# Optimization experiments

Measured on AMD Instinct MI355X. Metric: run time of the kernel, lower is better.

Reference implementation:

```python
import jax, jax.numpy as jnp
import numpy as np

F_FILT = 40      # num_filters
K_GABOR = 401    # n_coefficients
K_POOL = 401     # window_length
HOP = 160        # hop_length
SR = 16000
EPS_PCEN = 1e-6
EPS_IN = 1e-5    # nn.InstanceNorm1d default eps
B, T = 8, 160000


def _hz2mel(f):
    return 2595.0 * np.log10(1.0 + f / 700.0)


def _mel2hz(m):
    return 700.0 * (10.0 ** (m / 2595.0) - 1.0)


def setup_inputs() -> dict:
    key = jax.random.key(0)
    x = jax.random.normal(key, (B, 1, T), dtype=jnp.float32)
    # mel-spaced Gabor center frequencies / bandwidths (filter_init_method='mel')
    edges = _mel2hz(np.linspace(_hz2mel(60.0), _hz2mel(7800.0), F_FILT + 2))
    center = edges[1:-1]
    fwhm = np.maximum(edges[2:] - edges[:-2], 1.0)
    eta = 2.0 * np.pi * center / SR                      # rad/sample
    sigma = np.sqrt(2.0 * np.log(2.0)) / (np.pi * fwhm / SR)  # samples
    ones = jnp.ones(F_FILT, jnp.float32)
    return {
        "x": x,
        "gabor_eta": jnp.asarray(eta, jnp.float32),
        "gabor_sigma": jnp.asarray(sigma, jnp.float32),
        "pool_bandwidths": 0.4 * ones,   # GaussianLowPass init
        "pool_bias": ones,               # GaussianLowPass bias init (ones)
        "ema_weights": 0.04 * ones,      # sPCEN smoothing_coefficient, per-channel
        "alpha": 0.96 * ones,
        "delta": 2.0 * ones,
        "root": 0.96 * ones,             # root=compression_factor=0.96
    }


def _conv1d(x, w, stride=1, groups=1):
    # x: (N, C, T), w: (O, C//groups, K); cross-correlation like torch F.conv1d
    return jax.lax.conv_general_dilated(
        x, w, (stride,), "VALID",
        dimension_numbers=("NCH", "OIH", "NCH"),
        feature_group_count=groups)


def _ema_scan(x, s):
    # y_0 = x_0 ; y_t = s*x_t + (1-s)*y_{t-1}  (per-channel s), parallel scan
    s3 = s[None, :, None]
    a = jnp.broadcast_to(1.0 - s3, x.shape)
    b = s3 * x
    a = a.at[:, :, 0].set(0.0)
    b = b.at[:, :, 0].set(x[:, :, 0])
    def comb(c1, c2):
        a1, b1 = c1
        a2, b2 = c2
        return a1 * a2, a2 * b1 + b2
    _, y = jax.lax.associative_scan(comb, (a, b), axis=2)
    return y


def reference(x, gabor_eta, gabor_sigma, pool_bandwidths, pool_bias,
              ema_weights, alpha, delta, root):
    dt = x.dtype
    # --- Gabor complex conv frontend -> |.|^2 ---
    t = jnp.arange(K_GABOR, dtype=dt) - (K_GABOR - 1) / 2.0
    env = jnp.exp(-0.5 * (t[None] / gabor_sigma[:, None]) ** 2) \
          / (jnp.sqrt(2.0 * jnp.pi) * gabor_sigma[:, None])
    phase = gabor_eta[:, None] * t[None]
    kern = jnp.stack([env * jnp.cos(phase), env * jnp.sin(phase)], axis=1)
    kern = kern.reshape(2 * F_FILT, 1, K_GABOR)
    xp = jnp.pad(x, ((0, 0), (0, 0), (K_GABOR - 1, 0)))  # causal pad
    y = _conv1d(xp, kern)                                 # (B, 2F, T)
    y = y.reshape(y.shape[0], F_FILT, 2, y.shape[-1])
    power = y[:, :, 0] ** 2 + y[:, :, 1] ** 2             # |z|^2, (B, F, T)

    # --- sPCEN compression ---
    s = jnp.clip(ema_weights, 0.0, 1.0)
    ema = _ema_scan(power, s)
    a3 = jnp.minimum(alpha, 1.0)[None, :, None]
    inv_r = (1.0 / jnp.maximum(root, 1.0))[None, :, None]
    d3 = delta[None, :, None]
    comp = (power / (EPS_PCEN + ema) ** a3 + d3) ** inv_r - d3 ** inv_r

    # --- Gaussian low-pass depthwise pooling (causal, stride=HOP) ---
    bw = jnp.clip(pool_bandwidths, 2.0 / K_POOL, 0.5)
    tp = jnp.arange(-K_POOL // 2, K_POOL // 2, dtype=dt)  # -201..199, len 401
    den = bw * 0.5 * (K_POOL - 1)
    pk = jnp.exp(-0.5 * (tp[None] / den[:, None]) ** 2).reshape(F_FILT, 1, K_POOL)
    cp = jnp.pad(comp, ((0, 0), (0, 0), (K_POOL - 1, 0)))
    pooled = _conv1d(cp, pk, stride=HOP, groups=F_FILT) + pool_bias[None, :, None]

    # --- InstanceNorm1d (affine=False, biased var, eps=1e-5) ---
    m = pooled.mean(-1, keepdims=True)
    v = pooled.var(-1, keepdims=True)
    return (pooled - m) / jnp.sqrt(v + EPS_IN)
```

## Files before the change

### kernel.cpp

```cpp
#include <hip/hip_runtime.h>
#include <math.h>

#define F_FILT   40
#define K_GABOR  401
#define HOP      160
#define T_LEN    160000
#define B_BATCH  8
#define EPS_PCENF 1e-6f
#define EPS_INF   1e-5f

#define NG       5
#define GF       8
#define NKMAX    13
#define TC       640
#define UW       10
#define NCH1     250
#define NSTG     136
#define PHS      548

#define PC_THREADS 256
#define PC_NWAVES  4
#define SPAN     6400
#define W_NT     5
#define NSP      25
#define RT       20
#define KP       208
#define HALOP    200
#define RINGW    840
#define WSTR     1048

typedef _Float16 h2_t  __attribute__((ext_vector_type(2)));
typedef _Float16 half8 __attribute__((ext_vector_type(8)));
typedef float    f32x4 __attribute__((ext_vector_type(4)));

__device__ __forceinline__ float fdot2(h2_t a, h2_t b, float c) {
    return __builtin_amdgcn_fdot2(a, b, c, false);
}
__device__ __forceinline__ unsigned pk2(float a, float b) {
    return __builtin_bit_cast(unsigned, __builtin_amdgcn_cvt_pkrtz(a, b));
}
__device__ __forceinline__ h2_t bch(unsigned u) {
    return __builtin_bit_cast(h2_t, u);
}
__device__ __forceinline__ float fexp2(float x) { return __builtin_amdgcn_exp2f(x); }
__device__ __forceinline__ float flog2(float x) { return __builtin_amdgcn_logf(x); }

__device__ __forceinline__ void group_span(float sigma0, int& klo, int& nk) {
    const int R = min(200, (int)ceilf(4.0f * sigma0));
    klo = (200 - R) & ~31;
    nk  = ((200 + R - klo) >> 5) + 1;
    if (nk > NKMAX) nk = NKMAX;
}

__global__ __launch_bounds__(256) void leaf_weights(
    const float* __restrict__ eta_g, const float* __restrict__ sigma_g,
    const float* __restrict__ bw_g,
    _Float16* __restrict__ Atab, unsigned* __restrict__ pktab)
{
    const int gi = blockIdx.x;
    const int f0 = gi * GF;
    int klo, nk;
    group_span(sigma_g[f0], klo, nk);

    for (int idx = threadIdx.x; idx < 52 * 16 * 8; idx += 256) {
        const int c8 = idx >> 7;
        const int m  = (idx >> 3) & 15;
        const int i  = idx & 7;
        const int f  = f0 + (m >> 1);
        const int k  = klo + c8 * 8 + i;
        float w = 0.f;
        if (k <= 400) {
            const float sg = sigma_g[f];
            const float t  = (float)(k - 200);
            const float z  = t / sg;
            const float e  = (0.3989422804014327f / sg) * expf(-0.5f * z * z);
            const float ph = eta_g[f] * t;
            w = (m & 1) ? e * sinf(ph) : e * cosf(ph);
        }
        Atab[(size_t)(gi * 52 + c8) * 128 + m * 8 + i] = (_Float16)w;
    }
    for (int idx = threadIdx.x; idx < GF * KP; idx += 256) {
        const int fl = idx / KP, i = idx % KP;
        const int f = f0 + fl;
        const float bw  = fminf(fmaxf(bw_g[f], 2.0f / 401.0f), 0.5f);
        const float den = bw * 0.5f * 400.0f;
        float pp[2];
        for (int j = 0; j < 2; ++j) {
            int k = 2 * i + j;
            float pv = 0.f;
            if (k < K_GABOR) {
                float tp = (float)(k - 201);
                float d = tp / den;
                pv = expf(-0.5f * d * d);
            }
            pp[j] = pv;
        }
        pktab[f * KP + i] = pk2(pp[0], pp[1]);
    }
}

template<int NK>
__device__ __forceinline__ void conv_kloop(
    const uint4* __restrict__ ph4, const uint4* __restrict__ Ap,
    int aBase, int pbase, f32x4* acc)
{
    uint4 F[UW];
#pragma unroll
    for (int u = 0; u < UW; ++u) F[u] = ph4[pbase + 2 * u];
#pragma unroll
    for (int jk = 0; jk < NK; ++jk) {
        const half8 aCur = __builtin_bit_cast(half8, Ap[aBase + jk * 64]);
#pragma unroll
        for (int u = 0; u < UW; ++u) {
            acc[u] = __builtin_amdgcn_mfma_f32_16x16x32_f16(
                aCur, __builtin_bit_cast(half8, F[(2 * jk + u) % UW]), acc[u], 0, 0, 0);
        }
        if (jk + 1 < NK) {
            F[(2 * jk) % UW]     = ph4[pbase + 4 * (jk + 1) + 16];
            F[(2 * jk + 1) % UW] = ph4[pbase + 4 * (jk + 1) + 18];
        }
    }
}

__global__ __launch_bounds__(256) void leaf_conv(
    const float* __restrict__ x,
    const float* __restrict__ sigma_g,
    const _Float16* __restrict__ Atab,
    _Float16* __restrict__ Pall)
{
    __shared__ unsigned ph[8 * PHS];

    const int gi = blockIdx.x % NG;
    const int ch = (blockIdx.x / NG) % NCH1;
    const int b  = blockIdx.x / (NG * NCH1);
    const int f0 = gi * GF;
    const int tid = threadIdx.x;
    const int lane = tid & 63;
    const int w    = tid >> 6;

    const float* __restrict__ xb = x + (size_t)b * T_LEN;
    _Float16* __restrict__ Pb = Pall + (size_t)b * F_FILT * T_LEN;

    int klo, nk;
    group_span(sigma_g[f0], klo, nk);
    const int t0   = ch * TC;
    const int base = t0 + klo - 400;

    if (tid < NSTG) {
        const int g0 = base + 8 * tid;
        float v[15];
        if (g0 >= 0 && g0 + 14 < T_LEN) {
            const float4 a0 = *(const float4*)(xb + g0);
            const float4 a1 = *(const float4*)(xb + g0 + 4);
            const float4 a2 = *(const float4*)(xb + g0 + 8);
            const float4 a3 = *(const float4*)(xb + g0 + 12);
            v[0]=a0.x; v[1]=a0.y; v[2]=a0.z; v[3]=a0.w;
            v[4]=a1.x; v[5]=a1.y; v[6]=a1.z; v[7]=a1.w;
            v[8]=a2.x; v[9]=a2.y; v[10]=a2.z; v[11]=a2.w;
            v[12]=a3.x; v[13]=a3.y; v[14]=a3.z;
        } else {
#pragma unroll
            for (int e = 0; e < 15; ++e) {
                const int gidx = g0 + e;
                v[e] = (gidx >= 0 && gidx < T_LEN) ? xb[gidx] : 0.f;
            }
        }
        unsigned pw[14];
#pragma unroll
        for (int s = 0; s < 14; ++s) pw[s] = pk2(v[s], v[s + 1]);
#pragma unroll
        for (int r = 0; r < 8; ++r) {
            uint4 fr;
            fr.x = pw[r]; fr.y = pw[r + 2]; fr.z = pw[r + 4]; fr.w = pw[r + 6];
            *(uint4*)&ph[r * PHS + 4 * tid] = fr;
        }
    }
    __syncthreads();

    const int n  = lane & 15;
    const int kb = lane >> 4;
    const int q  = n + 8 * kb + 160 * w;
    const int pbase = (q & 7) * (PHS / 4) + (q >> 3);

    f32x4 acc[UW];
#pragma unroll
    for (int u = 0; u < UW; ++u) acc[u] = (f32x4){0.f, 0.f, 0.f, 0.f};

    const uint4* ph4 = (const uint4*)ph;
    const uint4* Ap = (const uint4*)Atab;
    const int aBase = (gi * 52 + kb) * 16 + n;

    switch (nk) {
        case 3:  conv_kloop<3>(ph4, Ap, aBase, pbase, acc); break;
        case 4:  conv_kloop<4>(ph4, Ap, aBase, pbase, acc); break;
        case 5:  conv_kloop<5>(ph4, Ap, aBase, pbase, acc); break;
        case 6:
        case 7:  conv_kloop<7>(ph4, Ap, aBase, pbase, acc); break;
        case 8:
        case 9:  conv_kloop<9>(ph4, Ap, aBase, pbase, acc); break;
        default: conv_kloop<13>(ph4, Ap, aBase, pbase, acc); break;
    }

    const int g  = lane >> 4;
    const int fA = f0 + 2 * g;
#pragma unroll
    for (int u = 0; u < UW; ++u) {
        const int t = t0 + (w * UW + u) * 16 + n;
        const float P0 = acc[u].x * acc[u].x + acc[u].y * acc[u].y;
        const float P1 = acc[u].z * acc[u].z + acc[u].w * acc[u].w;
        Pb[(size_t)fA * T_LEN + t]       = (_Float16)P0;
        Pb[(size_t)(fA + 1) * T_LEN + t] = (_Float16)P1;
    }
}

__global__ __launch_bounds__(PC_THREADS) void leaf_pcen(
    const _Float16* __restrict__ Pall,
    const float* __restrict__ bias_g,
    const float* __restrict__ ema_g,
    const float* __restrict__ alpha_g,
    const float* __restrict__ delta_g,
    const float* __restrict__ root_g,
    const unsigned* __restrict__ pktab,
    float* __restrict__ outp)
{
    __shared__ unsigned lds[PC_NWAVES * WSTR];

    const int tid  = threadIdx.x;
    const int lane = tid & 63;
    const int wv   = tid >> 6;
    const int wid  = blockIdx.x * PC_NWAVES + wv;
    const int sp   = wid % NSP;
    const int bf   = wid / NSP;
    const int f    = bf % F_FILT;

    unsigned* ring = lds + wv * WSTR;
    unsigned* pkl  = ring + RINGW;

    const float sw    = fminf(fmaxf(ema_g[f], 0.0f), 1.0f);
    const float a     = 1.0f - sw;
    const float alpha = fminf(alpha_g[f], 1.0f);
    const float inv_r = 1.0f / fmaxf(root_g[f], 1.0f);
    const float dlt   = delta_g[f];
    const float dpow  = fexp2(inv_r * flog2(dlt));
    const bool  rt1   = (inv_r == 1.0f);
    const float bias  = bias_g[f];

    for (int i = lane; i < KP; i += 64) pkl[i] = pktab[f * KP + i];
    for (int i = lane; i < HALOP; i += 64) ring[i] = 0u;

    const float a2 = a * a, a4 = a2 * a2, a8 = a4 * a4, a16 = a8 * a8;
    const float A1  = a16 * a4;
    const float A2  = A1 * A1, A4 = A2 * A2, A8 = A4 * A4;
    const float A16 = A8 * A8, A32 = A16 * A16, A64 = A32 * A32;
    float Al = 1.0f;
    if (lane & 1)  Al *= A1;
    if (lane & 2)  Al *= A2;
    if (lane & 4)  Al *= A4;
    if (lane & 8)  Al *= A8;
    if (lane & 16) Al *= A16;
    if (lane & 32) Al *= A32;

    const unsigned* PU = (const unsigned*)(Pall + (size_t)bf * T_LEN);
    const int wbase = sp * (SPAN / 2);
    const int itStart = (sp == 0) ? 0 : -1;
    float carry = 0.f;

    unsigned sv[10];
    {
        const int tb = wbase + itStart * 640 + lane * 10;
#pragma unroll
        for (int q = 0; q < 10; ++q) sv[q] = PU[tb + q];
    }

    for (int it = itStart; it < W_NT; ++it) {
        float p[RT];
#pragma unroll
        for (int q = 0; q < 10; ++q) {
            const h2_t hh = bch(sv[q]);
            p[2 * q]     = (float)hh.x;
            p[2 * q + 1] = (float)hh.y;
        }
        {
            const int nt = it + 1;
            const int tb = wbase + (nt < W_NT ? nt : 0) * 640 + lane * 10;
#pragma unroll
            for (int q = 0; q < 10; ++q) sv[q] = PU[tb + q];
        }

        float up[RT];
        float uu = 0.f;
#pragma unroll
        for (int r = 0; r < RT; ++r) {
            uu = fmaf(a, uu, sw * p[r]);
            up[r] = uu;
        }

        float cc = carry;
        if (sp == 0 && it == 0) cc = __shfl(p[0], 0);

        float v = uu;
        {
            float tv;
            tv = __shfl_up(v, 1);  if (lane >= 1)  v = fmaf(A1,  tv, v);
            tv = __shfl_up(v, 2);  if (lane >= 2)  v = fmaf(A2,  tv, v);
            tv = __shfl_up(v, 4);  if (lane >= 4)  v = fmaf(A4,  tv, v);
            tv = __shfl_up(v, 8);  if (lane >= 8)  v = fmaf(A8,  tv, v);
            tv = __shfl_up(v, 16); if (lane >= 16) v = fmaf(A16, tv, v);
            tv = __shfl_up(v, 32); if (lane >= 32) v = fmaf(A32, tv, v);
        }
        const float vlast = __shfl(v, 63);
        float cin;
        {
            float ve = __shfl_up(v, 1);
            if (lane == 0) ve = 0.f;
            cin = fmaf(Al, cc, ve);
        }
        carry = fmaf(A64, cc, vlast);

        float apr = a;
#pragma unroll
        for (int j = 0; j < 10; ++j) {
            const float e0 = fmaf(apr, cin, up[2 * j]);     apr *= a;
            const float e1 = fmaf(apr, cin, up[2 * j + 1]); apr *= a;
            const float d0 = fexp2(-alpha * flog2(EPS_PCENF + e0));
            const float d1 = fexp2(-alpha * flog2(EPS_PCENF + e1));
            float c0, c1;
            if (rt1) {
                c0 = p[2 * j] * d0;
                c1 = p[2 * j + 1] * d1;
            } else {
                const float q0 = fmaf(p[2 * j],     d0, dlt);
                const float q1 = fmaf(p[2 * j + 1], d1, dlt);
                c0 = fexp2(inv_r * flog2(q0)) - dpow;
                c1 = fexp2(inv_r * flog2(q1)) - dpow;
            }
            ring[HALOP + lane * 10 + j] = pk2(c0, c1);
        }

        if (it >= 0) {
            const int o = lane >> 3, l = lane & 7;
            float part = 0.f;
#pragma unroll
            for (int t = 0; t < 26; ++t) {
                const int kpp = l + 8 * t;
                part = fdot2(bch(ring[o * 80 + kpp]), bch(pkl[kpp]), part);
            }
            part += __shfl_xor(part, 1, 8);
            part += __shfl_xor(part, 2, 8);
            part += __shfl_xor(part, 4, 8);
            if (l == 0)
                outp[(size_t)bf * 1000 + sp * (W_NT * 8) + it * 8 + o] = part + bias;
        }

        if (lane < 50) {
            const uint4 hv = *(const uint4*)&ring[640 + 4 * lane];
            *(uint4*)&ring[4 * lane] = hv;
        }
    }
}

__global__ __launch_bounds__(256) void leaf_norm(float* __restrict__ out)
{
    const int bf = blockIdx.x;
    float* p = out + (size_t)bf * 1000;
    __shared__ float buf[1000];
    __shared__ float red[4];
    const int tid = threadIdx.x;
    const int lane = tid & 63, wave = tid >> 6;

    float sum = 0.0f;
    for (int i = tid; i < 1000; i += 256) { float v = p[i]; buf[i] = v; sum += v; }
    for (int m = 1; m < 64; m <<= 1) sum += __shfl_xor(sum, m);
    if (lane == 0) red[wave] = sum;
    __syncthreads();
    const float mean = (red[0] + red[1] + red[2] + red[3]) * 0.001f;

    float vs = 0.0f;
    for (int i = tid; i < 1000; i += 256) { float d = buf[i] - mean; vs += d * d; }
    for (int m = 1; m < 64; m <<= 1) vs += __shfl_xor(vs, m);
    __syncthreads();
    if (lane == 0) red[wave] = vs;
    __syncthreads();
    const float var   = (red[0] + red[1] + red[2] + red[3]) * 0.001f;
    const float scale = rsqrtf(var + EPS_INF);
    for (int i = tid; i < 1000; i += 256) p[i] = (buf[i] - mean) * scale;
}

extern "C" void kernel_launch(void* const* d_in, const int* in_sizes, int n_in,
                              void* d_out, int out_size, void* d_ws, size_t ws_size,
                              hipStream_t stream)
{
    const float* x     = (const float*)d_in[0];
    const float* eta   = (const float*)d_in[1];
    const float* sigma = (const float*)d_in[2];
    const float* bw    = (const float*)d_in[3];
    const float* bias  = (const float*)d_in[4];
    const float* emaw  = (const float*)d_in[5];
    const float* alpha = (const float*)d_in[6];
    const float* delta = (const float*)d_in[7];
    const float* root  = (const float*)d_in[8];
    float* outp = (float*)d_out;

    _Float16* Atab  = (_Float16*)d_ws;
    unsigned* pktab = (unsigned*)((char*)d_ws + 133120);
    _Float16* Pall  = (_Float16*)((char*)d_ws + 166400);

    hipLaunchKernelGGL(leaf_weights, dim3(NG), dim3(256), 0, stream,
                       eta, sigma, bw, Atab, pktab);
    hipLaunchKernelGGL(leaf_conv, dim3(B_BATCH * NG * NCH1), dim3(256), 0, stream,
                       x, sigma, Atab, Pall);
    hipLaunchKernelGGL(leaf_pcen, dim3(B_BATCH * F_FILT * NSP / PC_NWAVES), dim3(PC_THREADS),
                       0, stream, Pall, bias, emaw, alpha, delta, root, pktab, outp);
    hipLaunchKernelGGL(leaf_norm, dim3(B_BATCH * F_FILT), dim3(256), 0, stream, outp);
}
```

Measured before the change: 102.3 us.

## Fuse all filter groups into one conv block sharing staged input tile

After: 115.1 us. 1.13x slower.

```diff
diff --git a/kernel.cpp b/kernel.cpp
--- a/kernel.cpp
+++ b/kernel.cpp
@@ -11,12 +11,12 @@
 
 #define NG       5
 #define GF       8
-#define NKMAX    13
-#define TC       640
-#define UW       10
-#define NCH1     250
-#define NSTG     136
-#define PHS      548
+#define NCHK     13
+#define TC2      256
+#define UW2      4
+#define NCH2     625
+#define NSTG2    84
+#define PHS2     356
 
 #define PC_THREADS 256
 #define PC_NWAVES  4
@@ -49,7 +49,7 @@
     const int R = min(200, (int)ceilf(4.0f * sigma0));
     klo = (200 - R) & ~31;
     nk  = ((200 + R - klo) >> 5) + 1;
-    if (nk > NKMAX) nk = NKMAX;
+    if (nk > NCHK) nk = NCHK;
 }
 
 __global__ __launch_bounds__(256) void leaf_weights(
@@ -59,15 +59,13 @@
 {
     const int gi = blockIdx.x;
     const int f0 = gi * GF;
-    int klo, nk;
-    group_span(sigma_g[f0], klo, nk);
 
     for (int idx = threadIdx.x; idx < 52 * 16 * 8; idx += 256) {
         const int c8 = idx >> 7;
         const int m  = (idx >> 3) & 15;
         const int i  = idx & 7;
         const int f  = f0 + (m >> 1);
-        const int k  = klo + c8 * 8 + i;
+        const int k  = c8 * 8 + i;
         float w = 0.f;
         if (k <= 400) {
             const float sg = sigma_g[f];
@@ -99,41 +97,16 @@
     }
 }
 
-template<int NK>
-__device__ __forceinline__ void conv_kloop(
-    const uint4* __restrict__ ph4, const uint4* __restrict__ Ap,
-    int aBase, int pbase, f32x4* acc)
-{
-    uint4 F[UW];
-#pragma unroll
-    for (int u = 0; u < UW; ++u) F[u] = ph4[pbase + 2 * u];
-#pragma unroll
-    for (int jk = 0; jk < NK; ++jk) {
-        const half8 aCur = __builtin_bit_cast(half8, Ap[aBase + jk * 64]);
-#pragma unroll
-        for (int u = 0; u < UW; ++u) {
-            acc[u] = __builtin_amdgcn_mfma_f32_16x16x32_f16(
-                aCur, __builtin_bit_cast(half8, F[(2 * jk + u) % UW]), acc[u], 0, 0, 0);
-        }
-        if (jk + 1 < NK) {
-            F[(2 * jk) % UW]     = ph4[pbase + 4 * (jk + 1) + 16];
-            F[(2 * jk + 1) % UW] = ph4[pbase + 4 * (jk + 1) + 18];
-        }
-    }
-}
-
 __global__ __launch_bounds__(256) void leaf_conv(
     const float* __restrict__ x,
     const float* __restrict__ sigma_g,
     const _Float16* __restrict__ Atab,
     _Float16* __restrict__ Pall)
 {
-    __shared__ unsigned ph[8 * PHS];
-
-    const int gi = blockIdx.x % NG;
-    const int ch = (blockIdx.x / NG) % NCH1;
-    const int b  = blockIdx.x / (NG * NCH1);
-    const int f0 = gi * GF;
+    __shared__ unsigned ph[8 * PHS2];
+
+    const int ch = blockIdx.x % NCH2;
+    const int b  = blockIdx.x / NCH2;
     const int tid = threadIdx.x;
     const int lane = tid & 63;
     const int w    = tid >> 6;
@@ -141,12 +114,19 @@
     const float* __restrict__ xb = x + (size_t)b * T_LEN;
     _Float16* __restrict__ Pb = Pall + (size_t)b * F_FILT * T_LEN;
 
-    int klo, nk;
-    group_span(sigma_g[f0], klo, nk);
-    const int t0   = ch * TC;
-    const int base = t0 + klo - 400;
-
-    if (tid < NSTG) {
+    const int t0   = ch * TC2;
+    const int base = t0 - 400;
+
+    int c0g[NG], c1g[NG];
+#pragma unroll
+    for (int gi = 0; gi < NG; ++gi) {
+        int klo, nk;
+        group_span(sigma_g[gi * GF], klo, nk);
+        c0g[gi] = klo >> 5;
+        c1g[gi] = (klo >> 5) + nk;
+    }
+
+    if (tid < NSTG2) {
         const int g0 = base + 8 * tid;
         float v[15];
         if (g0 >= 0 && g0 + 14 < T_LEN) {
@@ -172,44 +152,72 @@
         for (int r = 0; r < 8; ++r) {
             uint4 fr;
             fr.x = pw[r]; fr.y = pw[r + 2]; fr.z = pw[r + 4]; fr.w = pw[r + 6];
-            *(uint4*)&ph[r * PHS + 4 * tid] = fr;
+            *(uint4*)&ph[r * PHS2 + 4 * tid] = fr;
         }
     }
     __syncthreads();
 
     const int n  = lane & 15;
     const int kb = lane >> 4;
-    const int q  = n + 8 * kb + 160 * w;
-    const int pbase = (q & 7) * (PHS / 4) + (q >> 3);
-
-    f32x4 acc[UW];
-#pragma unroll
-    for (int u = 0; u < UW; ++u) acc[u] = (f32x4){0.f, 0.f, 0.f, 0.f};
+    const int q  = n + 8 * kb + 64 * w;
+    const int pbase = (q & 7) * (PHS2 / 4) + (q >> 3);
+
+    f32x4 acc[NG][UW2];
+#pragma unroll
+    for (int gi = 0; gi < NG; ++gi)
+#pragma unroll
+        for (int u = 0; u < UW2; ++u) acc[gi][u] = (f32x4){0.f, 0.f, 0.f, 0.f};
 
     const uint4* ph4 = (const uint4*)ph;
-    const uint4* Ap = (const uint4*)Atab;
-    const int aBase = (gi * 52 + kb) * 16 + n;
-
-    switch (nk) {
-        case 3:  conv_kloop<3>(ph4, Ap, aBase, pbase, acc); break;
-        case 4:  conv_kloop<4>(ph4, Ap, aBase, pbase, acc); break;
-        case 5:  conv_kloop<5>(ph4, Ap, aBase, pbase, acc); break;
-        case 6:
-        case 7:  conv_kloop<7>(ph4, Ap, aBase, pbase, acc); break;
-        case 8:
-        case 9:  conv_kloop<9>(ph4, Ap, aBase, pbase, acc); break;
-        default: conv_kloop<13>(ph4, Ap, aBase, pbase, acc); break;
-    }
-
-    const int g  = lane >> 4;
-    const int fA = f0 + 2 * g;
-#pragma unroll
-    for (int u = 0; u < UW; ++u) {
-        const int t = t0 + (w * UW + u) * 16 + n;
-        const float P0 = acc[u].x * acc[u].x + acc[u].y * acc[u].y;
-        const float P1 = acc[u].z * acc[u].z + acc[u].w * acc[u].w;
-        Pb[(size_t)fA * T_LEN + t]       = (_Float16)P0;
-        Pb[(size_t)(fA + 1) * T_LEN + t] = (_Float16)P1;
+    const uint4* Ap  = (const uint4*)Atab;
+
+    uint4 F[UW2];
+#pragma unroll
+    for (int u = 0; u < UW2; ++u) F[u] = ph4[pbase + 2 * u];
+
+    uint4 aC[NG], aN[NG];
+#pragma unroll
+    for (int gi = 0; gi < NG; ++gi) aC[gi] = Ap[(gi * 52 + kb) * 16 + n];
+
+#pragma unroll
+    for (int jk = 0; jk < NCHK; ++jk) {
+        if (jk + 1 < NCHK) {
+#pragma unroll
+            for (int gi = 0; gi < NG; ++gi)
+                aN[gi] = Ap[(gi * 52 + 4 * (jk + 1) + kb) * 16 + n];
+        }
+#pragma unroll
+        for (int gi = 0; gi < NG; ++gi) {
+            if (jk >= c0g[gi] && jk < c1g[gi]) {
+                const half8 aCur = __builtin_bit_cast(half8, aC[gi]);
+#pragma unroll
+                for (int u = 0; u < UW2; ++u) {
+                    acc[gi][u] = __builtin_amdgcn_mfma_f32_16x16x32_f16(
+                        aCur, __builtin_bit_cast(half8, F[(2 * jk + u) & 3]),
+                        acc[gi][u], 0, 0, 0);
+                }
+            }
+        }
+        if (jk + 1 < NCHK) {
+            F[(2 * (jk + 1) + 2) & 3] = ph4[pbase + 4 * (jk + 1) + 4];
+            F[(2 * (jk + 1) + 3) & 3] = ph4[pbase + 4 * (jk + 1) + 6];
+#pragma unroll
+            for (int gi = 0; gi < NG; ++gi) aC[gi] = aN[gi];
+        }
+    }
+
+    const int g = lane >> 4;
+#pragma unroll
+    for (int gi = 0; gi < NG; ++gi) {
+        const int fA = gi * GF + 2 * g;
+#pragma unroll
+        for (int u = 0; u < UW2; ++u) {
+            const int t = t0 + (w * UW2 + u) * 16 + n;
+            const float P0 = acc[gi][u].x * acc[gi][u].x + acc[gi][u].y * acc[gi][u].y;
+            const float P1 = acc[gi][u].z * acc[gi][u].z + acc[gi][u].w * acc[gi][u].w;
+            Pb[(size_t)fA * T_LEN + t]       = (_Float16)P0;
+            Pb[(size_t)(fA + 1) * T_LEN + t] = (_Float16)P1;
+        }
     }
 }
 
@@ -407,7 +415,7 @@
 
     hipLaunchKernelGGL(leaf_weights, dim3(NG), dim3(256), 0, stream,
                        eta, sigma, bw, Atab, pktab);
-    hipLaunchKernelGGL(leaf_conv, dim3(B_BATCH * NG * NCH1), dim3(256), 0, stream,
+    hipLaunchKernelGGL(leaf_conv, dim3(B_BATCH * NCH2), dim3(256), 0, stream,
                        x, sigma, Atab, Pall);
     hipLaunchKernelGGL(leaf_pcen, dim3(B_BATCH * F_FILT * NSP / PC_NWAVES), dim3(PC_THREADS),
                        0, stream, Pall, bias, emaw, alpha, delta, root, pktab, outp);
```
